# Optimization experiments

Measured on AMD Instinct MI355X. Metric: run time of the kernel, lower is better.

Reference implementation:

```python
import jax, jax.numpy as jnp
import numpy as np

L = 5        # num GNN layers
H = 256      # hidden size
N = 200000   # total nodes in batch
E = 400000   # total edges
G = 8000     # number of graphs (25 nodes each)


def _gelu(x):
    return jax.nn.gelu(x, approximate=False)


def _ln(x, g, b, eps=1e-5):
    m = x.mean(-1, keepdims=True)
    v = ((x - m) ** 2).mean(-1, keepdims=True)
    return (x - m) / jnp.sqrt(v + eps) * g + b


def _mlp(x, w1, b1, g, bb, w2, b2):
    # Linear -> LayerNorm -> GELU -> Linear (dropout is identity in eval)
    h = x @ w1 + b1
    h = _ln(h, g, bb)
    h = _gelu(h)
    return h @ w2 + b2


def setup_inputs() -> dict:
    key = jax.random.key(0)
    ks = jax.random.split(key, 24)
    s = 0.02
    inp = {}
    inp['x'] = jax.random.randint(ks[0], (N,), 0, 118)
    inp['edge_index'] = jax.random.randint(ks[1], (2, E), 0, N)
    inp['edge_attr'] = jax.random.randint(ks[2], (E,), 0, 5)
    # deterministic sorted graph ids: 25 nodes per graph, all G graphs nonempty
    inp['batch'] = jnp.arange(N, dtype=jnp.int32) // (N // G)
    # embeddings
    inp['atom_emb'] = jax.random.normal(ks[3], (118, H), jnp.float32) * s
    inp['vn_emb'] = jnp.zeros((1, H), jnp.float32)  # init constant 0
    inp['bond_emb'] = jax.random.normal(ks[4], (L, 5, H), jnp.float32) * s
    inp['eps'] = jnp.zeros((L,), jnp.float32)
    # GINConv mlp params (stacked over layers)
    inp['c_w1'] = jax.random.normal(ks[5], (L, H, 4 * H), jnp.float32) * s
    inp['c_b1'] = jnp.zeros((L, 4 * H), jnp.float32)
    inp['c_lng'] = jnp.ones((L, 4 * H), jnp.float32)
    inp['c_lnb'] = jnp.zeros((L, 4 * H), jnp.float32)
    inp['c_w2'] = jax.random.normal(ks[6], (L, 4 * H, H), jnp.float32) * s
    inp['c_b2'] = jnp.zeros((L, H), jnp.float32)
    # per-layer output LayerNorms
    inp['n_g'] = jnp.ones((L, H), jnp.float32)
    inp['n_b'] = jnp.zeros((L, H), jnp.float32)
    # virtual-node MLPs (L-1 of them)
    inp['v_w1'] = jax.random.normal(ks[7], (L - 1, H, 4 * H), jnp.float32) * s
    inp['v_b1'] = jnp.zeros((L - 1, 4 * H), jnp.float32)
    inp['v_lng'] = jnp.ones((L - 1, 4 * H), jnp.float32)
    inp['v_lnb'] = jnp.zeros((L - 1, 4 * H), jnp.float32)
    inp['v_w2'] = jax.random.normal(ks[8], (L - 1, 4 * H, H), jnp.float32) * s
    inp['v_b2'] = jnp.zeros((L - 1, H), jnp.float32)
    # projection head
    inp['p_w1'] = jax.random.normal(ks[9], (H, H), jnp.float32) * s
    inp['p_b1'] = jnp.zeros((H,), jnp.float32)
    inp['p_lng'] = jnp.ones((H,), jnp.float32)
    inp['p_lnb'] = jnp.zeros((H,), jnp.float32)
    inp['p_w2'] = jax.random.normal(ks[10], (H, H), jnp.float32) * s
    inp['p_b2'] = jnp.zeros((H,), jnp.float32)
    return inp


def reference(x, edge_index, edge_attr, batch, atom_emb, vn_emb, bond_emb, eps,
              c_w1, c_b1, c_lng, c_lnb, c_w2, c_b2, n_g, n_b,
              v_w1, v_b1, v_lng, v_lnb, v_w2, v_b2,
              p_w1, p_b1, p_lng, p_lnb, p_w2, p_b2):
    src, dst = edge_index[0], edge_index[1]
    vn = jnp.broadcast_to(vn_emb[0], (G, H))  # virtualnode embedding per graph
    h = atom_emb[x]                            # [N, H]
    for l in range(L):
        h = h + vn[batch]
        h_in = h
        # GINConv: gather + add + gelu per edge, scatter-add at dst
        edge_e = bond_emb[l][edge_attr]        # [E, H]
        msg = _gelu(h[src] + edge_e)           # [E, H]
        aggr = jax.ops.segment_sum(msg, dst, num_segments=N)
        out = _mlp((1.0 + eps[l]) * h + aggr,
                   c_w1[l], c_b1[l], c_lng[l], c_lnb[l], c_w2[l], c_b2[l])
        out = _ln(out, n_g[l], n_b[l])
        if l < L - 1:
            out = _gelu(out)
        h = out + h_in                         # residual
        if l < L - 1:
            vp = jax.ops.segment_max(h_in, batch, num_segments=G)
            vn = vn + _mlp(vp, v_w1[l], v_b1[l], v_lng[l], v_lnb[l], v_w2[l], v_b2[l])
    h_graph = jax.ops.segment_sum(h, batch, num_segments=G)  # [G, H]
    z = h_graph @ p_w1 + p_b1
    z = _gelu(_ln(z, p_lng, p_lnb))
    z = z @ p_w2 + p_b2
    z = z / jnp.linalg.norm(z, axis=-1, keepdims=True)
    return z
```

## Files before the change

### kernel.cpp

```cpp
#include <hip/hip_runtime.h>
#include <math.h>

typedef __bf16 bf16_t;
typedef __bf16 bfrag  __attribute__((ext_vector_type(8)));
typedef __bf16 b4     __attribute__((ext_vector_type(4)));
typedef __bf16 b2v    __attribute__((ext_vector_type(2)));
typedef float  f32x4  __attribute__((ext_vector_type(4)));

static constexpr int LY  = 5;
static constexpr int H   = 256;
static constexpr int NN  = 200000;
static constexpr int EE  = 400000;
static constexpr int GG  = 8000;
static constexpr int NPG = 25;
static constexpr int CAP = 24;
static constexpr int NBLK_NODE = NN / 32;
static constexpr int NBLK_VN   = GG / 32;

__device__ __forceinline__ float gelu_f(float x) {
    const float y = 0.7978845608028654f * x * (1.0f + 0.044715f * x * x);
    const float e = __expf(2.0f * y);
    const float t = 1.0f - 2.0f / (e + 1.0f);
    return 0.5f * x * (1.0f + t);
}

__global__ void k_fill(float* __restrict__ out, float v, int n) {
    const int i = blockIdx.x * 256 + threadIdx.x;
    if (i < n) out[i] = v;
}

__global__ void k_detect(const void* __restrict__ probe, int* __restrict__ flag) {
    const bf16_t* p = (const bf16_t*)probe;
    int bad = 0;
    for (int i = threadIdx.x; i < 256; i += 64) {
        const float v = (float)p[i];
        if (!(v == v) || fabsf(v) > 1000.0f) bad = 1;
    }
    const int any = __any(bad) ? 1 : 0;
    if (threadIdx.x == 0) *flag = any;
}

struct CvtJobs {
    const void* src[18];
    bf16_t*     dst[18];
    int         pfx[19];
    int         njobs;
};
__global__ void k_cvt_all(CvtJobs J, const int* __restrict__ flag) {
    const int i = blockIdx.x * 256 + threadIdx.x;
    if (i >= J.pfx[J.njobs]) return;
    int j = 0;
    while (i >= J.pfx[j + 1]) ++j;
    const int loc = i - J.pfx[j];
    if (*flag) J.dst[j][loc] = (bf16_t)((const float*)J.src[j])[loc];
    else       J.dst[j][loc] = ((const bf16_t*)J.src[j])[loc];
}

struct TpJobs {
    const void* s32[22];
    const void* s16[22];
    bf16_t*     dst[22];
    int R[22], C[22];
    int pfx[23];
    int njobs;
};
__global__ void k_tp_all(TpJobs J, const int* __restrict__ flag) {
    __shared__ bf16_t t[32][33];
    const int tile = blockIdx.x;
    int j = 0;
    while (tile >= J.pfx[j + 1]) ++j;
    const int tl = tile - J.pfx[j];
    const int C = J.C[j], R = J.R[j];
    const int ntx = C / 32;
    const int c0 = (tl % ntx) * 32, r0 = (tl / ntx) * 32;
    const int f = *flag;
    const int tx = threadIdx.x & 31, ty = threadIdx.x >> 5;
    #pragma unroll
    for (int i = 0; i < 4; ++i) {
        const int r = ty + i * 8;
        const size_t idx = (size_t)(r0 + r) * C + c0 + tx;
        t[r][tx] = f ? (bf16_t)((const float*)J.s32[j])[idx] : ((const bf16_t*)J.s16[j])[idx];
    }
    __syncthreads();
    #pragma unroll
    for (int i = 0; i < 4; ++i) {
        const int r = ty + i * 8;
        J.dst[j][(size_t)(c0 + r) * R + r0 + tx] = t[tx][r];
    }
}

__global__ void k_init_h(const int* __restrict__ x, const bf16_t* __restrict__ atom,
                         bf16_t* __restrict__ h) {
    const size_t idx = (size_t)blockIdx.x * 256 + threadIdx.x;
    const int row = (int)(idx >> 8), col = (int)(idx & 255);
    h[idx] = atom[(size_t)x[row] * H + col];
}

__global__ void k_init_vn(const bf16_t* __restrict__ vne, float* __restrict__ vn) {
    const size_t idx = (size_t)blockIdx.x * 256 + threadIdx.x;
    vn[idx] = (float)vne[idx & 255];
}

__global__ void k_zero_cnt(int* __restrict__ cnt) {
    const int i = blockIdx.x * 256 + threadIdx.x;
    if (i < NN) cnt[i] = 0;
}
// ... 2 lines not shown
                         int* __restrict__ cnt, int* __restrict__ slots) {
    const int e = blockIdx.x * 256 + threadIdx.x;
    if (e >= EE) return;
    const int d = ei[EE + e];
    const int s = ei[e];
    const int a = ea[e];
    const int slot = atomicAdd(&cnt[d], 1);
    if (slot < CAP) slots[(size_t)d * CAP + slot] = s | (a << 18);
}

__global__ void k_addvn_segmax(bf16_t* __restrict__ h, const float* __restrict__ vn,
                               bf16_t* __restrict__ vp, int do_max) {
    const int g = blockIdx.x, t = threadIdx.x;
    const float2 v = *(const float2*)(vn + (size_t)g * H + 2 * t);
    float mx0 = -1e30f, mx1 = -1e30f;
    #pragma unroll 5
    for (int i = 0; i < NPG; ++i) {
        bf16_t* p = h + ((size_t)g * NPG + i) * H + 2 * t;
        const b2v hv = *(const b2v*)p;
        const float h0 = (float)hv[0] + v.x;
        const float h1 = (float)hv[1] + v.y;
        b2v o; o[0] = (bf16_t)h0; o[1] = (bf16_t)h1;
        *(b2v*)p = o;
        mx0 = fmaxf(mx0, h0); mx1 = fmaxf(mx1, h1);
    }
    if (do_max) {
        b2v o; o[0] = (bf16_t)mx0; o[1] = (bf16_t)mx1;
        *(b2v*)(vp + (size_t)g * H + 2 * t) = o;
    }
}

__global__ void k_gather(const bf16_t* __restrict__ h,
                         const bf16_t* __restrict__ bondl,
                         const int* __restrict__ cnt, const int* __restrict__ slots,
                         const bf16_t* __restrict__ epsb, int l, bf16_t* __restrict__ Xb) {
    const int n = blockIdx.x, t = threadIdx.x;
    int deg = cnt[n];
    if (deg > CAP) deg = CAP;
    float m0 = 0.0f, m1 = 0.0f;
    for (int i = 0; i < deg; ++i) {
        const int p = slots[(size_t)n * CAP + i];
        const int s = p & 0x3FFFF;
        const int a = p >> 18;
        const b2v hv = *(const b2v*)(h + (size_t)s * H + 2 * t);
        const b2v bv = *(const b2v*)(bondl + (size_t)a * H + 2 * t);
        m0 += gelu_f((float)hv[0] + (float)bv[0]);
        m1 += gelu_f((float)hv[1] + (float)bv[1]);
    }
    const float eps1 = 1.0f + (float)epsb[l];
    const b2v hn = *(const b2v*)(h + (size_t)n * H + 2 * t);
    b2v o;
    o[0] = (bf16_t)(eps1 * (float)hn[0] + m0);
    o[1] = (bf16_t)(eps1 * (float)hn[1] + m1);
    *(b2v*)(Xb + (size_t)n * H + 2 * t) = o;
}

__global__ void k_graphsum(const bf16_t* __restrict__ h, bf16_t* __restrict__ hg) {
    const int g = blockIdx.x, t = threadIdx.x;
    float s0 = 0.0f, s1 = 0.0f;
    #pragma unroll 5
    for (int i = 0; i < NPG; ++i) {
        const b2v hv = *(const b2v*)(h + ((size_t)g * NPG + i) * H + 2 * t);
        s0 += (float)hv[0]; s1 += (float)hv[1];
    }
    b2v o; o[0] = (bf16_t)s0; o[1] = (bf16_t)s1;
    *(b2v*)(hg + (size_t)g * H + 2 * t) = o;
}

__global__ void k_norm(const float* __restrict__ z, float* __restrict__ out) {
    const int row = blockIdx.x, t = threadIdx.x;
    const size_t idx = (size_t)row * H + t;
    const float v = z[idx];
    float q = v * v;
    #pragma unroll
    for (int o = 32; o > 0; o >>= 1) q += __shfl_xor(q, o, 64);
    __shared__ float rq[4];
    const int wave = t >> 6, lane = t & 63;
    if (lane == 0) rq[wave] = q;
    __syncthreads();
    q = rq[0] + rq[1] + rq[2] + rq[3];
    out[idx] = v * rsqrtf(q);
}

__launch_bounds__(512, 4)
__global__ void k_mlp_dual(const bf16_t* __restrict__ Xn, const bf16_t* __restrict__ Xv,
                           const bf16_t* __restrict__ nW1T, const bf16_t* __restrict__ vW1T,
                           const bf16_t* __restrict__ nb1, const bf16_t* __restrict__ vb1,
                           const bf16_t* __restrict__ nlng, const bf16_t* __restrict__ vlng,
                           const bf16_t* __restrict__ nlnb, const bf16_t* __restrict__ vlnb,
                           const bf16_t* __restrict__ nW2T, const bf16_t* __restrict__ vW2T,
                           const bf16_t* __restrict__ nb2, const bf16_t* __restrict__ vb2,
                           const bf16_t* __restrict__ g2, const bf16_t* __restrict__ b2ln,
                           bf16_t* __restrict__ hres, float* __restrict__ vnacc,
                           int gelu_flag, int nblk_node, int has_vn) {
    constexpr int HID = 1024;
    constexpr int NP1 = HID / 128;
    constexpr int NQ2 = HID / 64;
    __shared__ bf16_t hid[32 * HID];
    __shared__ bf16_t wbuf[8192];
    const int tid  = threadIdx.x;
    const int lane = tid & 63, wave = tid >> 6;
    const int c16  = lane & 15, quad = lane >> 4;

    const bool is_node = (int)blockIdx.x < nblk_node;
    const size_t rowblk = is_node ? (size_t)blockIdx.x * 32
                                  : (size_t)((int)blockIdx.x - nblk_node) * 32;
    const bf16_t* X    = is_node ? Xn   : Xv;
    const bf16_t* W1T  = is_node ? nW1T : vW1T;
    const bf16_t* W2T  = is_node ? nW2T : vW2T;
    const bf16_t* b1   = is_node ? nb1  : vb1;
    const bf16_t* lng  = is_node ? nlng : vlng;
    const bf16_t* lnb  = is_node ? nlnb : vlnb;
    const bf16_t* b2   = is_node ? nb2  : vb2;

    auto stage = [&](const bf16_t* WT, int KW, int colbase, int k0) {
        #pragma unroll
        for (int j = 0; j < 2; ++j) {
            const int grp    = wave * 2 + j;
            const int colrel = grp * 8 + (lane >> 3);
            const int slot   = lane & 7;
            const int kq     = slot ^ (colrel & 7);
            const bf16_t* gp = WT + (size_t)(colbase + colrel) * KW + k0 + kq * 8;
            bf16_t* lp = &wbuf[(size_t)grp * 512];
            __builtin_amdgcn_global_load_lds(
                (const __attribute__((address_space(1))) void*)gp,
                (__attribute__((address_space(3))) void*)lp, 16, 0, 0);
        }
    };
    auto wfrag = [&](int crel, int g) -> bfrag {
        return *(const bfrag*)(wbuf + crel * 64 + ((g ^ (crel & 7)) * 8));
    };

    const bf16_t* xr0 = X + (rowblk + c16) * 256 + quad * 8;
    const bf16_t* xr1 = X + (rowblk + 16 + c16) * 256 + quad * 8;
    bfrag xa[8][2];
    #pragma unroll
    for (int ks = 0; ks < 8; ++ks) {
        xa[ks][0] = *(const bfrag*)(xr0 + ks * 32);
        xa[ks][1] = *(const bfrag*)(xr1 + ks * 32);
    }

    #pragma unroll
    for (int c = 0; c < NP1; ++c) {
        const int nbase = c * 128 + wave * 16;
        f32x4 acc[2];
        acc[0] = f32x4{0.f, 0.f, 0.f, 0.f};
        acc[1] = f32x4{0.f, 0.f, 0.f, 0.f};
        #pragma unroll
        for (int kc = 0; kc < 4; ++kc) {
            stage(W1T, 256, c * 128, kc * 64);
            __syncthreads();
            #pragma unroll
            for (int s = 0; s < 2; ++s) {
                const int ks = kc * 2 + s;
                const int g  = s * 4 + quad;
                const bfrag w0 = wfrag(wave * 16 + c16, g);
                #pragma unroll
                for (int mt = 0; mt < 2; ++mt)
                    acc[mt] = __builtin_amdgcn_mfma_f32_16x16x32_bf16(
                        w0, xa[ks][mt], acc[mt], 0, 0, 0);
            }
            __syncthreads();
        }
        #pragma unroll
        for (int mt = 0; mt < 2; ++mt) {
            const int kb = nbase + quad * 4;
            const int xr = mt * 16 + c16;
            const b4 bias = *(const b4*)(b1 + kb);
            b4 o;
            #pragma unroll
            for (int r = 0; r < 4; ++r)
                o[r] = (bf16_t)(acc[mt][r] + (float)bias[r]);
            const int ch = ((kb >> 3) ^ (xr & 7));
            *(b4*)(hid + xr * HID + ch * 8 + (kb & 7)) = o;
        }
    }
    __syncthreads();

    {
        const int row = tid >> 4, p = tid & 15;
        float sum = 0.f, ss = 0.f;
        #pragma unroll
        for (int i = 0; i < HID / 128; ++i) {
            const int j0 = p * 8 + i * 128;
            const int ch = ((j0 >> 3) ^ (row & 7));
            bfrag v = *(const bfrag*)(hid + row * HID + ch * 8);
            #pragma unroll
            for (int k = 0; k < 8; ++k) { const float f = (float)v[k]; sum += f; ss += f * f; }
        }
        #pragma unroll
        for (int o = 1; o < 16; o <<= 1) { sum += __shfl_xor(sum, o, 64); ss += __shfl_xor(ss, o, 64); }
        const float mean = sum * (1.0f / HID);
        const float var  = ss * (1.0f / HID) - mean * mean;
        const float rinv = rsqrtf(var + 1e-5f);
        #pragma unroll
        for (int i = 0; i < HID / 128; ++i) {
            const int j0 = p * 8 + i * 128;
            const int ch = ((j0 >> 3) ^ (row & 7));
            bfrag v  = *(const bfrag*)(hid + row * HID + ch * 8);
            bfrag gv = *(const bfrag*)(lng + j0);
            bfrag bv = *(const bfrag*)(lnb + j0);
            bfrag o8;
            #pragma unroll
            for (int k = 0; k < 8; ++k) {
                const float f = ((float)v[k] - mean) * rinv * (float)gv[k] + (float)bv[k];
                o8[k] = (bf16_t)gelu_f(f);
            }
            *(bfrag*)(hid + row * HID + ch * 8) = o8;
        }
    }
    __syncthreads();

    {
        f32x4 acc2[2][2];
        #pragma unroll
        for (int cp = 0; cp < 2; ++cp)
            #pragma unroll
            for (int mt = 0; mt < 2; ++mt)
                acc2[cp][mt] = f32x4{0.f, 0.f, 0.f, 0.f};
        #pragma unroll
        for (int cp = 0; cp < 2; ++cp) {
            for (int q2 = 0; q2 < NQ2; ++q2) {
                stage(W2T, HID, cp * 128, q2 * 64);
                __syncthreads();
                #pragma unroll
                for (int s = 0; s < 2; ++s) {
                    const int g = s * 4 + quad;
                    const bfrag w0 = wfrag(wave * 16 + c16, g);
                    const int k = q2 * 64 + s * 32 + quad * 8;
                    bfrag hb[2];
                    #pragma unroll
                    for (int mt = 0; mt < 2; ++mt) {
                        const int row = mt * 16 + c16;
                        const int ch = ((k >> 3) ^ (row & 7));
                        hb[mt] = *(const bfrag*)(hid + row * HID + ch * 8);
                    }
                    #pragma unroll
                    for (int mt = 0; mt < 2; ++mt)
                        acc2[cp][mt] = __builtin_amdgcn_mfma_f32_16x16x32_bf16(
                            w0, hb[mt], acc2[cp][mt], 0, 0, 0);
                }
                __syncthreads();
            }
        }

        if (!is_node) {
            if (has_vn) {
                #pragma unroll
                for (int cp = 0; cp < 2; ++cp)
                    #pragma unroll
                    for (int mt = 0; mt < 2; ++mt) {
                        const int cb = cp * 128 + wave * 16 + quad * 4;
                        const b4 b2vv = *(const b4*)(b2 + cb);
                        float* po = vnacc + (rowblk + mt * 16 + c16) * 256 + cb;
                        const f32x4 old = *(const f32x4*)po;
                        f32x4 v;
                        #pragma unroll
                        for (int r = 0; r < 4; ++r) v[r] = old[r] + acc2[cp][mt][r] + (float)b2vv[r];
                        *(f32x4*)po = v;
                    }
            }
        } else {
            constexpr int OS = 260;
            float* ot = (float*)hid;
            __syncthreads();
            #pragma unroll
            for (int cp = 0; cp < 2; ++cp)
                #pragma unroll
                for (int mt = 0; mt < 2; ++mt) {
                    const int cb = cp * 128 + wave * 16 + quad * 4;
                    const b4 b2vv = *(const b4*)(b2 + cb);
                    f32x4 v;
                    #pragma unroll
                    for (int r = 0; r < 4; ++r) v[r] = acc2[cp][mt][r] + (float)b2vv[r];
                    *(f32x4*)(ot + (mt * 16 + c16) * OS + cb) = v;
                }
            __syncthreads();
            const int row = tid >> 4, p = tid & 15;
            float s = 0.f, q = 0.f;
            #pragma unroll
            for (int i = 0; i < 16; ++i) {
                const float f = ot[row * OS + p + 16 * i];
                s += f; q += f * f;
            }
            #pragma unroll
            for (int o = 1; o < 16; o <<= 1) { s += __shfl_xor(s, o, 64); q += __shfl_xor(q, o, 64); }
            const float mean = s * (1.0f / 256.0f);
            const float var  = q * (1.0f / 256.0f) - mean * mean;
            const float rinv = rsqrtf(var + 1e-5f);
            const size_t rg = (rowblk + row) * 256;
            #pragma unroll
            for (int i = 0; i < 2; ++i) {
                const int j0 = p * 16 + i * 8;
                bfrag gv = *(const bfrag*)(g2 + j0);
                bfrag bv = *(const bfrag*)(b2ln + j0);
                bfrag hv = *(const bfrag*)(hres + rg + j0);
                bfrag o8;
                #pragma unroll
                for (int k = 0; k < 8; ++k) {
                    float f = (ot[row * OS + j0 + k] - mean) * rinv * (float)gv[k] + (float)bv[k];
                    if (gelu_flag) f = gelu_f(f);
                    o8[k] = (bf16_t)(f + (float)hv[k]);
                }
                *(bfrag*)(hres + rg + j0) = o8;
            }
        }
    }
}

__launch_bounds__(512, 4)
__global__ void k_mlp_proj(const bf16_t* __restrict__ X, const bf16_t* __restrict__ W1T,
                           const bf16_t* __restrict__ b1, const bf16_t* __restrict__ lng,
                           const bf16_t* __restrict__ lnb, const bf16_t* __restrict__ W2T,
                           const bf16_t* __restrict__ b2, float* __restrict__ outf) {
    constexpr int HID = 256;
    constexpr int NP1 = HID / 128;
    constexpr int NQ2 = HID / 64;
    __shared__ bf16_t hid[32 * HID];
    __shared__ bf16_t wbuf[8192];
    const int tid  = threadIdx.x;
    const int lane = tid & 63, wave = tid >> 6;
    const int c16  = lane & 15, quad = lane >> 4;
    const size_t rowblk = (size_t)blockIdx.x * 32;

    auto stage = [&](const bf16_t* WT, int KW, int colbase, int k0) {
        #pragma unroll
        for (int j = 0; j < 2; ++j) {
            const int grp    = wave * 2 + j;
            const int colrel = grp * 8 + (lane >> 3);
            const int slot   = lane & 7;
            const int kq     = slot ^ (colrel & 7);
            const bf16_t* gp = WT + (size_t)(colbase + colrel) * KW + k0 + kq * 8;
            bf16_t* lp = &wbuf[(size_t)grp * 512];
            __builtin_amdgcn_global_load_lds(
                (const __attribute__((address_space(1))) void*)gp,
                (__attribute__((address_space(3))) void*)lp, 16, 0, 0);
        }
    };
    auto wfrag = [&](int crel, int g) -> bfrag {
        return *(const bfrag*)(wbuf + crel * 64 + ((g ^ (crel & 7)) * 8));
    };

    const bf16_t* xr0 = X + (rowblk + c16) * 256 + quad * 8;
    const bf16_t* xr1 = X + (rowblk + 16 + c16) * 256 + quad * 8;
    bfrag xa[8][2];
    #pragma unroll
    for (int ks = 0; ks < 8; ++ks) {
        xa[ks][0] = *(const bfrag*)(xr0 + ks * 32);
        xa[ks][1] = *(const bfrag*)(xr1 + ks * 32);
    }

    #pragma unroll
    for (int c = 0; c < NP1; ++c) {
        const int nbase = c * 128 + wave * 16;
        f32x4 acc[2];
        acc[0] = f32x4{0.f, 0.f, 0.f, 0.f};
        acc[1] = f32x4{0.f, 0.f, 0.f, 0.f};
        #pragma unroll
        for (int kc = 0; kc < 4; ++kc) {
            stage(W1T, 256, c * 128, kc * 64);
            __syncthreads();
            #pragma unroll
            for (int s = 0; s < 2; ++s) {
                const int ks = kc * 2 + s;
                const int g  = s * 4 + quad;
                const bfrag w0 = wfrag(wave * 16 + c16, g);
                #pragma unroll
                for (int mt = 0; mt < 2; ++mt)
                    acc[mt] = __builtin_amdgcn_mfma_f32_16x16x32_bf16(
                        w0, xa[ks][mt], acc[mt], 0, 0, 0);
            }
            __syncthreads();
        }
        #pragma unroll
        for (int mt = 0; mt < 2; ++mt) {
            const int kb = nbase + quad * 4;
            const int xr = mt * 16 + c16;
            const b4 bias = *(const b4*)(b1 + kb);
            b4 o;
            #pragma unroll
            for (int r = 0; r < 4; ++r)
                o[r] = (bf16_t)(acc[mt][r] + (float)bias[r]);
            const int ch = ((kb >> 3) ^ (xr & 7));
            *(b4*)(hid + xr * HID + ch * 8 + (kb & 7)) = o;
        }
    }
    __syncthreads();

    {
        const int row = tid >> 4, p = tid & 15;
        float sum = 0.f, ss = 0.f;
        #pragma unroll
        for (int i = 0; i < HID / 128; ++i) {
            const int j0 = p * 8 + i * 128;
            const int ch = ((j0 >> 3) ^ (row & 7));
            bfrag v = *(const bfrag*)(hid + row * HID + ch * 8);
            #pragma unroll
            for (int k = 0; k < 8; ++k) { const float f = (float)v[k]; sum += f; ss += f * f; }
        }
        #pragma unroll
        for (int o = 1; o < 16; o <<= 1) { sum += __shfl_xor(sum, o, 64); ss += __shfl_xor(ss, o, 64); }
        const float mean = sum * (1.0f / HID);
        const float var  = ss * (1.0f / HID) - mean * mean;
        const float rinv = rsqrtf(var + 1e-5f);
        #pragma unroll
        for (int i = 0; i < HID / 128; ++i) {
            const int j0 = p * 8 + i * 128;
            const int ch = ((j0 >> 3) ^ (row & 7));
            bfrag v  = *(const bfrag*)(hid + row * HID + ch * 8);
            bfrag gv = *(const bfrag*)(lng + j0);
            bfrag bv = *(const bfrag*)(lnb + j0);
            bfrag o8;
            #pragma unroll
            for (int k = 0; k < 8; ++k) {
                const float f = ((float)v[k] - mean) * rinv * (float)gv[k] + (float)bv[k];
                o8[k] = (bf16_t)gelu_f(f);
            }
            *(bfrag*)(hid + row * HID + ch * 8) = o8;
        }
    }
    __syncthreads();

    {
        f32x4 acc2[2][2];
        #pragma unroll
        for (int cp = 0; cp < 2; ++cp)
            #pragma unroll
            for (int mt = 0; mt < 2; ++mt)
                acc2[cp][mt] = f32x4{0.f, 0.f, 0.f, 0.f};
        #pragma unroll
        for (int cp = 0; cp < 2; ++cp) {
            for (int q2 = 0; q2 < NQ2; ++q2) {
                stage(W2T, HID, cp * 128, q2 * 64);
                __syncthreads();
                #pragma unroll
                for (int s = 0; s < 2; ++s) {
                    const int g = s * 4 + quad;
                    const bfrag w0 = wfrag(wave * 16 + c16, g);
                    const int k = q2 * 64 + s * 32 + quad * 8;
                    bfrag hb[2];
                    #pragma unroll
                    for (int mt = 0; mt < 2; ++mt) {
                        const int row = mt * 16 + c16;
                        const int ch = ((k >> 3) ^ (row & 7));
                        hb[mt] = *(const bfrag*)(hid + row * HID + ch * 8);
                    }
                    #pragma unroll
                    for (int mt = 0; mt < 2; ++mt)
                        acc2[cp][mt] = __builtin_amdgcn_mfma_f32_16x16x32_bf16(
                            w0, hb[mt], acc2[cp][mt], 0, 0, 0);
                }
                __syncthreads();
            }
        }
        #pragma unroll
        for (int cp = 0; cp < 2; ++cp)
            #pragma unroll
            for (int mt = 0; mt < 2; ++mt) {
                const int cb = cp * 128 + wave * 16 + quad * 4;
                const b4 b2vv = *(const b4*)(b2 + cb);
                f32x4 v;
                #pragma unroll
                for (int r = 0; r < 4; ++r) v[r] = acc2[cp][mt][r] + (float)b2vv[r];
                *(f32x4*)(outf + (rowblk + mt * 16 + c16) * 256 + cb) = v;
            }
    }
}

extern "C" void kernel_launch(void* const* d_in, const int* in_sizes, int n_in,
                              void* d_out, int out_size, void* d_ws, size_t ws_size,
                              hipStream_t stream) {
    float* outz = (float*)d_out;

    const bool layout_ok =
        (n_in == 28) &&
        in_sizes[0] == 200000 && in_sizes[1] == 800000 &&
        in_sizes[2] == 400000 && in_sizes[3] == 200000 &&
        in_sizes[4] == 118 * 256 && in_sizes[6] == 5 * 5 * 256 &&
        in_sizes[8] == 5 * 256 * 1024 && in_sizes[27] == 256 &&
        out_size == GG * H;
    if (!layout_ok) {
        k_fill<<<(out_size + 255) / 256, 256, 0, stream>>>(outz, 777.0f, out_size);
        return;
    }

    char* w = (char*)d_ws;
    size_t off = 0;
    auto alloc = [&](size_t bytes) -> void* {
        void* p = w + off;
        off += (bytes + 255) & ~(size_t)255;
        return p;
    };
    bf16_t* h     = (bf16_t*)alloc((size_t)NN * H * 2);
    bf16_t* Xb    = (bf16_t*)alloc((size_t)NN * H * 2);
    float*  vn    = (float*) alloc((size_t)GG * H * 4);
    bf16_t* vpb   = (bf16_t*)alloc((size_t)GG * H * 2);
    bf16_t* hgb   = (bf16_t*)alloc((size_t)GG * H * 2);
    float*  pout2 = (float*) alloc((size_t)GG * H * 4);
    int*    cnt   = (int*)   alloc((size_t)NN * 4);
    int*    slots = (int*)   alloc((size_t)NN * CAP * 4);
    int*    dflag = (int*)   alloc(256);
    bf16_t* cw1T  = (bf16_t*)alloc((size_t)LY * 1024 * 256 * 2);
    bf16_t* cw2T  = (bf16_t*)alloc((size_t)LY * 256 * 1024 * 2);
    bf16_t* vw1T  = (bf16_t*)alloc((size_t)(LY - 1) * 1024 * 256 * 2);
    bf16_t* vw2T  = (bf16_t*)alloc((size_t)(LY - 1) * 256 * 1024 * 2);
    bf16_t* pw1T  = (bf16_t*)alloc((size_t)256 * 256 * 2);
    bf16_t* pw2T  = (bf16_t*)alloc((size_t)256 * 256 * 2);
    bf16_t* atomA = (bf16_t*)alloc((size_t)118 * 256 * 2);
    bf16_t* vneA  = (bf16_t*)alloc(256 * 2);
    bf16_t* bondA = (bf16_t*)alloc((size_t)LY * 5 * 256 * 2);
    bf16_t* epsA  = (bf16_t*)alloc(16 * 2);
    bf16_t* cb1A  = (bf16_t*)alloc((size_t)LY * 1024 * 2);
    bf16_t* clngA = (bf16_t*)alloc((size_t)LY * 1024 * 2);
    bf16_t* clnbA = (bf16_t*)alloc((size_t)LY * 1024 * 2);
    bf16_t* cb2A  = (bf16_t*)alloc((size_t)LY * 256 * 2);
    bf16_t* ngA   = (bf16_t*)alloc((size_t)LY * 256 * 2);
    bf16_t* nbA   = (bf16_t*)alloc((size_t)LY * 256 * 2);
    bf16_t* vb1A  = (bf16_t*)alloc((size_t)(LY - 1) * 1024 * 2);
    bf16_t* vlngA = (bf16_t*)alloc((size_t)(LY - 1) * 1024 * 2);
    bf16_t* vlnbA = (bf16_t*)alloc((size_t)(LY - 1) * 1024 * 2);
    bf16_t* vb2A  = (bf16_t*)alloc((size_t)(LY - 1) * 256 * 2);
    bf16_t* pb1A  = (bf16_t*)alloc(256 * 2);
    bf16_t* plngA = (bf16_t*)alloc(256 * 2);
    bf16_t* plnbA = (bf16_t*)alloc(256 * 2);
    bf16_t* pb2A  = (bf16_t*)alloc(256 * 2);
    if (off > ws_size) {
        k_fill<<<(out_size + 255) / 256, 256, 0, stream>>>(outz, 333.0f, out_size);
        return;
    }

    const int* xi  = (const int*)d_in[0];
    const int* ei  = (const int*)d_in[1];
    const int* ea  = (const int*)d_in[2];

    k_detect<<<1, 64, 0, stream>>>(d_in[8], dflag);
// ... 77 lines not shown
```

Measured before the change: 4.093 ms.

## Load MLP weight fragments directly from global memory instead of staging through LDS

In both fused MLP kernels, each wave now reads its MFMA weight fragments straight from global memory (L2/L1-cached) rather than cooperatively staging 64-wide K slices into an LDS buffer. This removes the per-slice __syncthreads pairs and frees 16KB of shared memory per block, which can allow higher occupancy. In exchange, each wave issues uncoalesced 16-byte global loads with exposed latency and no cross-wave sharing through LDS, so performance now depends on cache hit rates for the weights.

```diff
diff --git a/kernel.cpp b/kernel.cpp
--- a/kernel.cpp
+++ b/kernel.cpp
@@ -203,9 +203,7 @@
                            int gelu_flag, int nblk_node, int has_vn) {
     constexpr int HID = 1024;
     constexpr int NP1 = HID / 128;
-    constexpr int NQ2 = HID / 64;
     __shared__ bf16_t hid[32 * HID];
-    __shared__ bf16_t wbuf[8192];
     const int tid  = threadIdx.x;
     const int lane = tid & 63, wave = tid >> 6;
     const int c16  = lane & 15, quad = lane >> 4;
@@ -221,24 +219,6 @@
     const bf16_t* lnb  = is_node ? nlnb : vlnb;
     const bf16_t* b2   = is_node ? nb2  : vb2;
 
-    auto stage = [&](const bf16_t* WT, int KW, int colbase, int k0) {
-        #pragma unroll
-        for (int j = 0; j < 2; ++j) {
-            const int grp    = wave * 2 + j;
-            const int colrel = grp * 8 + (lane >> 3);
-            const int slot   = lane & 7;
-            const int kq     = slot ^ (colrel & 7);
-            const bf16_t* gp = WT + (size_t)(colbase + colrel) * KW + k0 + kq * 8;
-            bf16_t* lp = &wbuf[(size_t)grp * 512];
-            __builtin_amdgcn_global_load_lds(
-                (const __attribute__((address_space(1))) void*)gp,
-                (__attribute__((address_space(3))) void*)lp, 16, 0, 0);
-        }
-    };
-    auto wfrag = [&](int crel, int g) -> bfrag {
-        return *(const bfrag*)(wbuf + crel * 64 + ((g ^ (crel & 7)) * 8));
-    };
-
     const bf16_t* xr0 = X + (rowblk + c16) * 256 + quad * 8;
     const bf16_t* xr1 = X + (rowblk + 16 + c16) * 256 + quad * 8;
     bfrag xa[8][2];
@@ -248,39 +228,33 @@
         xa[ks][1] = *(const bfrag*)(xr1 + ks * 32);
     }
 
-    #pragma unroll
-    for (int c = 0; c < NP1; ++c) {
-        const int nbase = c * 128 + wave * 16;
-        f32x4 acc[2];
-        acc[0] = f32x4{0.f, 0.f, 0.f, 0.f};
-        acc[1] = f32x4{0.f, 0.f, 0.f, 0.f};
-        #pragma unroll
-        for (int kc = 0; kc < 4; ++kc) {
-            stage(W1T, 256, c * 128, kc * 64);
-            __syncthreads();
-            #pragma unroll
-            for (int s = 0; s < 2; ++s) {
-                const int ks = kc * 2 + s;
-                const int g  = s * 4 + quad;
-                const bfrag w0 = wfrag(wave * 16 + c16, g);
-                #pragma unroll
-                for (int mt = 0; mt < 2; ++mt)
-                    acc[mt] = __builtin_amdgcn_mfma_f32_16x16x32_bf16(
-                        w0, xa[ks][mt], acc[mt], 0, 0, 0);
-            }
-            __syncthreads();
-        }
-        #pragma unroll
-        for (int mt = 0; mt < 2; ++mt) {
-            const int kb = nbase + quad * 4;
-            const int xr = mt * 16 + c16;
-            const b4 bias = *(const b4*)(b1 + kb);
-            b4 o;
-            #pragma unroll
-            for (int r = 0; r < 4; ++r)
-                o[r] = (bf16_t)(acc[mt][r] + (float)bias[r]);
-            const int ch = ((kb >> 3) ^ (xr & 7));
-            *(b4*)(hid + xr * HID + ch * 8 + (kb & 7)) = o;
+    {
+        const bf16_t* w1l = W1T + (size_t)(wave * 16 + c16) * 256 + quad * 8;
+        #pragma unroll
+        for (int c = 0; c < NP1; ++c) {
+            const bf16_t* wp = w1l + (size_t)c * 128 * 256;
+            f32x4 acc[2];
+            acc[0] = f32x4{0.f, 0.f, 0.f, 0.f};
+            acc[1] = f32x4{0.f, 0.f, 0.f, 0.f};
+            #pragma unroll
+            for (int ks = 0; ks < 8; ++ks) {
+                const bfrag w0 = *(const bfrag*)(wp + ks * 32);
+                acc[0] = __builtin_amdgcn_mfma_f32_16x16x32_bf16(w0, xa[ks][0], acc[0], 0, 0, 0);
+                acc[1] = __builtin_amdgcn_mfma_f32_16x16x32_bf16(w0, xa[ks][1], acc[1], 0, 0, 0);
+            }
+            const int nbase = c * 128 + wave * 16;
+            #pragma unroll
+            for (int mt = 0; mt < 2; ++mt) {
+                const int kb = nbase + quad * 4;
+                const int xr = mt * 16 + c16;
+                const b4 bias = *(const b4*)(b1 + kb);
+                b4 o;
+                #pragma unroll
+                for (int r = 0; r < 4; ++r)
+                    o[r] = (bf16_t)(acc[mt][r] + (float)bias[r]);
+                const int ch = ((kb >> 3) ^ (xr & 7));
+                *(b4*)(hid + xr * HID + ch * 8 + (kb & 7)) = o;
+            }
         }
     }
     __syncthreads();
@@ -326,29 +300,25 @@
             #pragma unroll
             for (int mt = 0; mt < 2; ++mt)
                 acc2[cp][mt] = f32x4{0.f, 0.f, 0.f, 0.f};
+        const bf16_t* w2l = W2T + (size_t)(wave * 16 + c16) * HID + quad * 8;
         #pragma unroll
         for (int cp = 0; cp < 2; ++cp) {
-            for (int q2 = 0; q2 < NQ2; ++q2) {
-                stage(W2T, HID, cp * 128, q2 * 64);
-                __syncthreads();
-                #pragma unroll
-                for (int s = 0; s < 2; ++s) {
-                    const int g = s * 4 + quad;
-                    const bfrag w0 = wfrag(wave * 16 + c16, g);
-                    const int k = q2 * 64 + s * 32 + quad * 8;
-                    bfrag hb[2];
-                    #pragma unroll
-                    for (int mt = 0; mt < 2; ++mt) {
-                        const int row = mt * 16 + c16;
-                        const int ch = ((k >> 3) ^ (row & 7));
-                        hb[mt] = *(const bfrag*)(hid + row * HID + ch * 8);
-                    }
-                    #pragma unroll
-                    for (int mt = 0; mt < 2; ++mt)
-                        acc2[cp][mt] = __builtin_amdgcn_mfma_f32_16x16x32_bf16(
-                            w0, hb[mt], acc2[cp][mt], 0, 0, 0);
+            const bf16_t* wp = w2l + (size_t)cp * 128 * HID;
+            #pragma unroll 4
+            for (int kt = 0; kt < HID / 32; ++kt) {
+                const bfrag w0 = *(const bfrag*)(wp + kt * 32);
+                const int k = kt * 32 + quad * 8;
+                bfrag hb[2];
+                #pragma unroll
+                for (int mt = 0; mt < 2; ++mt) {
+                    const int row = mt * 16 + c16;
+                    const int ch = ((k >> 3) ^ (row & 7));
+                    hb[mt] = *(const bfrag*)(hid + row * HID + ch * 8);
                 }
-                __syncthreads();
+                #pragma unroll
+                for (int mt = 0; mt < 2; ++mt)
+                    acc2[cp][mt] = __builtin_amdgcn_mfma_f32_16x16x32_bf16(
+                        w0, hb[mt], acc2[cp][mt], 0, 0, 0);
             }
         }
 
@@ -423,31 +393,11 @@
                            const bf16_t* __restrict__ b2, float* __restrict__ outf) {
     constexpr int HID = 256;
     constexpr int NP1 = HID / 128;
-    constexpr int NQ2 = HID / 64;
     __shared__ bf16_t hid[32 * HID];
-    __shared__ bf16_t wbuf[8192];
     const int tid  = threadIdx.x;
     const int lane = tid & 63, wave = tid >> 6;
     const int c16  = lane & 15, quad = lane >> 4;
     const size_t rowblk = (size_t)blockIdx.x * 32;
-
-    auto stage = [&](const bf16_t* WT, int KW, int colbase, int k0) {
-        #pragma unroll
-        for (int j = 0; j < 2; ++j) {
-            const int grp    = wave * 2 + j;
-            const int colrel = grp * 8 + (lane >> 3);
-            const int slot   = lane & 7;
-            const int kq     = slot ^ (colrel & 7);
-            const bf16_t* gp = WT + (size_t)(colbase + colrel) * KW + k0 + kq * 8;
-            bf16_t* lp = &wbuf[(size_t)grp * 512];
-            __builtin_amdgcn_global_load_lds(
-                (const __attribute__((address_space(1))) void*)gp,
-                (__attribute__((address_space(3))) void*)lp, 16, 0, 0);
-        }
-    };
-    auto wfrag = [&](int crel, int g) -> bfrag {
-        return *(const bfrag*)(wbuf + crel * 64 + ((g ^ (crel & 7)) * 8));
-    };
 
     const bf16_t* xr0 = X + (rowblk + c16) * 256 + quad * 8;
     const bf16_t* xr1 = X + (rowblk + 16 + c16) * 256 + quad * 8;
@@ -458,39 +408,33 @@
         xa[ks][1] = *(const bfrag*)(xr1 + ks * 32);
     }
 
-    #pragma unroll
-    for (int c = 0; c < NP1; ++c) {
-        const int nbase = c * 128 + wave * 16;
-        f32x4 acc[2];
-        acc[0] = f32x4{0.f, 0.f, 0.f, 0.f};
-        acc[1] = f32x4{0.f, 0.f, 0.f, 0.f};
-        #pragma unroll
-        for (int kc = 0; kc < 4; ++kc) {
-            stage(W1T, 256, c * 128, kc * 64);
-            __syncthreads();
-            #pragma unroll
-            for (int s = 0; s < 2; ++s) {
-                const int ks = kc * 2 + s;
-                const int g  = s * 4 + quad;
-                const bfrag w0 = wfrag(wave * 16 + c16, g);
-                #pragma unroll
-                for (int mt = 0; mt < 2; ++mt)
-                    acc[mt] = __builtin_amdgcn_mfma_f32_16x16x32_bf16(
-                        w0, xa[ks][mt], acc[mt], 0, 0, 0);
-            }
-            __syncthreads();
-        }
-        #pragma unroll
-        for (int mt = 0; mt < 2; ++mt) {
-            const int kb = nbase + quad * 4;
-            const int xr = mt * 16 + c16;
-            const b4 bias = *(const b4*)(b1 + kb);
-            b4 o;
-            #pragma unroll
-            for (int r = 0; r < 4; ++r)
-                o[r] = (bf16_t)(acc[mt][r] + (float)bias[r]);
-            const int ch = ((kb >> 3) ^ (xr & 7));
-            *(b4*)(hid + xr * HID + ch * 8 + (kb & 7)) = o;
+    {
+        const bf16_t* w1l = W1T + (size_t)(wave * 16 + c16) * 256 + quad * 8;
+        #pragma unroll
+        for (int c = 0; c < NP1; ++c) {
+            const bf16_t* wp = w1l + (size_t)c * 128 * 256;
+            f32x4 acc[2];
+            acc[0] = f32x4{0.f, 0.f, 0.f, 0.f};
+            acc[1] = f32x4{0.f, 0.f, 0.f, 0.f};
+            #pragma unroll
+            for (int ks = 0; ks < 8; ++ks) {
+                const bfrag w0 = *(const bfrag*)(wp + ks * 32);
+                acc[0] = __builtin_amdgcn_mfma_f32_16x16x32_bf16(w0, xa[ks][0], acc[0], 0, 0, 0);
+                acc[1] = __builtin_amdgcn_mfma_f32_16x16x32_bf16(w0, xa[ks][1], acc[1], 0, 0, 0);
+            }
+            const int nbase = c * 128 + wave * 16;
+            #pragma unroll
+            for (int mt = 0; mt < 2; ++mt) {
+                const int kb = nbase + quad * 4;
+                const int xr = mt * 16 + c16;
+                const b4 bias = *(const b4*)(b1 + kb);
+                b4 o;
+                #pragma unroll
+                for (int r = 0; r < 4; ++r)
+                    o[r] = (bf16_t)(acc[mt][r] + (float)bias[r]);
+                const int ch = ((kb >> 3) ^ (xr & 7));
+                *(b4*)(hid + xr * HID + ch * 8 + (kb & 7)) = o;
+            }
         }
     }
     __syncthreads();
@@ -536,29 +480,25 @@
             #pragma unroll
             for (int mt = 0; mt < 2; ++mt)
                 acc2[cp][mt] = f32x4{0.f, 0.f, 0.f, 0.f};
+        const bf16_t* w2l = W2T + (size_t)(wave * 16 + c16) * HID + quad * 8;
         #pragma unroll
         for (int cp = 0; cp < 2; ++cp) {
-            for (int q2 = 0; q2 < NQ2; ++q2) {
-                stage(W2T, HID, cp * 128, q2 * 64);
-                __syncthreads();
-                #pragma unroll
-                for (int s = 0; s < 2; ++s) {
-                    const int g = s * 4 + quad;
-                    const bfrag w0 = wfrag(wave * 16 + c16, g);
-                    const int k = q2 * 64 + s * 32 + quad * 8;
-                    bfrag hb[2];
-                    #pragma unroll
-                    for (int mt = 0; mt < 2; ++mt) {
-                        const int row = mt * 16 + c16;
-                        const int ch = ((k >> 3) ^ (row & 7));
-                        hb[mt] = *(const bfrag*)(hid + row * HID + ch * 8);
-                    }
-                    #pragma unroll
-                    for (int mt = 0; mt < 2; ++mt)
-                        acc2[cp][mt] = __builtin_amdgcn_mfma_f32_16x16x32_bf16(
-                            w0, hb[mt], acc2[cp][mt], 0, 0, 0);
+            const bf16_t* wp = w2l + (size_t)cp * 128 * HID;
+            #pragma unroll
+            for (int kt = 0; kt < HID / 32; ++kt) {
+                const bfrag w0 = *(const bfrag*)(wp + kt * 32);
+                const int k = kt * 32 + quad * 8;
+                bfrag hb[2];
+                #pragma unroll
+                for (int mt = 0; mt < 2; ++mt) {
+                    const int row = mt * 16 + c16;
+                    const int ch = ((k >> 3) ^ (row & 7));
+                    hb[mt] = *(const bfrag*)(hid + row * HID + ch * 8);
                 }
-                __syncthreads();
+                #pragma unroll
+                for (int mt = 0; mt < 2; ++mt)
+                    acc2[cp][mt] = __builtin_amdgcn_mfma_f32_16x16x32_bf16(
+                        w0, hb[mt], acc2[cp][mt], 0, 0, 0);
             }
         }
         #pragma unroll
```

New measurement: 5.559 ms. 1.36x slower.

## Software-pipeline weight staging in dual MLP kernel with 4-deep LDS ring

Applied to the files above, without the earlier changes.

Replaces the single weight staging buffer and the two block barriers per k-chunk with a 4-slot LDS ring. Each round prefetches two rounds ahead with global_load_lds and uses one barrier gated by a partial vmcnt wait. Weight loads for W1 and W2 now overlap the MFMA work, and half the barriers disappear. Shared memory per block rises from 80 KB to 128 KB and launch bounds drop to 2 blocks per CU, which lowers occupancy. Relying on raw vmcnt counts for correctness is fragile, since the compiler may emit other vector memory ops that change the counts.

```diff
diff --git a/kernel.cpp b/kernel.cpp
--- a/kernel.cpp
+++ b/kernel.cpp
@@ -22,6 +22,31 @@
     const float e = __expf(2.0f * y);
     const float t = 1.0f - 2.0f / (e + 1.0f);
     return 0.5f * x * (1.0f + t);
+}
+
+__device__ __forceinline__ void pipe_bar_v4() {
+    asm volatile("s_waitcnt vmcnt(4)" ::: "memory");
+    __builtin_amdgcn_sched_barrier(0);
+    __builtin_amdgcn_s_barrier();
+    __builtin_amdgcn_sched_barrier(0);
+}
+__device__ __forceinline__ void pipe_bar_v2() {
+    asm volatile("s_waitcnt vmcnt(2)" ::: "memory");
+    __builtin_amdgcn_sched_barrier(0);
+    __builtin_amdgcn_s_barrier();
+    __builtin_amdgcn_sched_barrier(0);
+}
+__device__ __forceinline__ void pipe_bar_v0() {
+    asm volatile("s_waitcnt vmcnt(0)" ::: "memory");
+    __builtin_amdgcn_sched_barrier(0);
+    __builtin_amdgcn_s_barrier();
+    __builtin_amdgcn_sched_barrier(0);
+}
+__device__ __forceinline__ void lds_bar() {
+    asm volatile("s_waitcnt lgkmcnt(0)" ::: "memory");
+    __builtin_amdgcn_sched_barrier(0);
+    __builtin_amdgcn_s_barrier();
+    __builtin_amdgcn_sched_barrier(0);
 }
 
 __global__ void k_fill(float* __restrict__ out, float v, int n) {
@@ -190,7 +215,7 @@
     out[idx] = v * rsqrtf(q);
 }
 
-__launch_bounds__(512, 4)
+__launch_bounds__(512, 2)
 __global__ void k_mlp_dual(const bf16_t* __restrict__ Xn, const bf16_t* __restrict__ Xv,
                            const bf16_t* __restrict__ nW1T, const bf16_t* __restrict__ vW1T,
                            const bf16_t* __restrict__ nb1, const bf16_t* __restrict__ vb1,
@@ -202,10 +227,8 @@
                            bf16_t* __restrict__ hres, float* __restrict__ vnacc,
                            int gelu_flag, int nblk_node, int has_vn) {
     constexpr int HID = 1024;
-    constexpr int NP1 = HID / 128;
-    constexpr int NQ2 = HID / 64;
-    __shared__ bf16_t hid[32 * HID];
-    __shared__ bf16_t wbuf[8192];
+    __shared__ __align__(16) bf16_t hid[32 * HID];
+    __shared__ __align__(16) bf16_t wbuf[4][8192];
     const int tid  = threadIdx.x;
     const int lane = tid & 63, wave = tid >> 6;
     const int c16  = lane & 15, quad = lane >> 4;
@@ -221,7 +244,7 @@
     const bf16_t* lnb  = is_node ? nlnb : vlnb;
     const bf16_t* b2   = is_node ? nb2  : vb2;
 
-    auto stage = [&](const bf16_t* WT, int KW, int colbase, int k0) {
+    auto stage_to = [&](const bf16_t* WT, int KW, int colbase, int k0, bf16_t* lpbase) {
         #pragma unroll
         for (int j = 0; j < 2; ++j) {
             const int grp    = wave * 2 + j;
@@ -229,14 +252,20 @@
             const int slot   = lane & 7;
             const int kq     = slot ^ (colrel & 7);
             const bf16_t* gp = WT + (size_t)(colbase + colrel) * KW + k0 + kq * 8;
-            bf16_t* lp = &wbuf[(size_t)grp * 512];
+            bf16_t* lp = lpbase + (size_t)grp * 512;
             __builtin_amdgcn_global_load_lds(
                 (const __attribute__((address_space(1))) void*)gp,
                 (__attribute__((address_space(3))) void*)lp, 16, 0, 0);
         }
     };
-    auto wfrag = [&](int crel, int g) -> bfrag {
-        return *(const bfrag*)(wbuf + crel * 64 + ((g ^ (crel & 7)) * 8));
+    auto stage_round = [&](int g) {
+        bf16_t* base = wbuf[g & 3];
+        if (g < 32) {
+            stage_to(W1T, 256, (g >> 2) * 128, (g & 3) * 64, base);
+        } else {
+            const int gg = g - 32;
+            stage_to(W2T, HID, (gg >> 4) * 128, (gg & 15) * 64, base);
+        }
     };
 
     const bf16_t* xr0 = X + (rowblk + c16) * 256 + quad * 8;
@@ -248,28 +277,31 @@
         xa[ks][1] = *(const bfrag*)(xr1 + ks * 32);
     }
 
+    stage_round(0);
+    stage_round(1);
+
     #pragma unroll
-    for (int c = 0; c < NP1; ++c) {
-        const int nbase = c * 128 + wave * 16;
+    for (int c = 0; c < 8; ++c) {
         f32x4 acc[2];
         acc[0] = f32x4{0.f, 0.f, 0.f, 0.f};
         acc[1] = f32x4{0.f, 0.f, 0.f, 0.f};
         #pragma unroll
         for (int kc = 0; kc < 4; ++kc) {
-            stage(W1T, 256, c * 128, kc * 64);
-            __syncthreads();
+            const int r = c * 4 + kc;
+            stage_round(r + 2);
+            pipe_bar_v4();
+            const bf16_t* sb = wbuf[r & 3];
             #pragma unroll
             for (int s = 0; s < 2; ++s) {
                 const int ks = kc * 2 + s;
-                const int g  = s * 4 + quad;
-                const bfrag w0 = wfrag(wave * 16 + c16, g);
-                #pragma unroll
-                for (int mt = 0; mt < 2; ++mt)
-                    acc[mt] = __builtin_amdgcn_mfma_f32_16x16x32_bf16(
-                        w0, xa[ks][mt], acc[mt], 0, 0, 0);
-            }
-            __syncthreads();
-        }
+                const int gq = s * 4 + quad;
+                const int crel = wave * 16 + c16;
+                const bfrag w0 = *(const bfrag*)(sb + crel * 64 + ((gq ^ (crel & 7)) * 8));
+                acc[0] = __builtin_amdgcn_mfma_f32_16x16x32_bf16(w0, xa[ks][0], acc[0], 0, 0, 0);
+                acc[1] = __builtin_amdgcn_mfma_f32_16x16x32_bf16(w0, xa[ks][1], acc[1], 0, 0, 0);
+            }
+        }
+        const int nbase = c * 128 + wave * 16;
         #pragma unroll
         for (int mt = 0; mt < 2; ++mt) {
             const int kb = nbase + quad * 4;
@@ -283,7 +315,7 @@
             *(b4*)(hid + xr * HID + ch * 8 + (kb & 7)) = o;
         }
     }
-    __syncthreads();
+    lds_bar();
 
     {
         const int row = tid >> 4, p = tid & 15;
@@ -317,7 +349,7 @@
             *(bfrag*)(hid + row * HID + ch * 8) = o8;
         }
     }
-    __syncthreads();
+    lds_bar();
 
     {
         f32x4 acc2[2][2];
@@ -328,13 +360,19 @@
                 acc2[cp][mt] = f32x4{0.f, 0.f, 0.f, 0.f};
         #pragma unroll
         for (int cp = 0; cp < 2; ++cp) {
-            for (int q2 = 0; q2 < NQ2; ++q2) {
-                stage(W2T, HID, cp * 128, q2 * 64);
-                __syncthreads();
+            #pragma unroll
+            for (int q2 = 0; q2 < 16; ++q2) {
+                const int g = 32 + cp * 16 + q2;
+                if (g + 2 <= 63) stage_round(g + 2);
+                if (g <= 61)      pipe_bar_v4();
+                else if (g == 62) pipe_bar_v2();
+                else              pipe_bar_v0();
+                const bf16_t* sb = wbuf[g & 3];
                 #pragma unroll
                 for (int s = 0; s < 2; ++s) {
-                    const int g = s * 4 + quad;
-                    const bfrag w0 = wfrag(wave * 16 + c16, g);
+                    const int gq = s * 4 + quad;
+                    const int crel = wave * 16 + c16;
+                    const bfrag w0 = *(const bfrag*)(sb + crel * 64 + ((gq ^ (crel & 7)) * 8));
                     const int k = q2 * 64 + s * 32 + quad * 8;
                     bfrag hb[2];
                     #pragma unroll
@@ -343,12 +381,9 @@
                         const int ch = ((k >> 3) ^ (row & 7));
                         hb[mt] = *(const bfrag*)(hid + row * HID + ch * 8);
                     }
-                    #pragma unroll
-                    for (int mt = 0; mt < 2; ++mt)
-                        acc2[cp][mt] = __builtin_amdgcn_mfma_f32_16x16x32_bf16(
-                            w0, hb[mt], acc2[cp][mt], 0, 0, 0);
+                    acc2[cp][0] = __builtin_amdgcn_mfma_f32_16x16x32_bf16(w0, hb[0], acc2[cp][0], 0, 0, 0);
+                    acc2[cp][1] = __builtin_amdgcn_mfma_f32_16x16x32_bf16(w0, hb[1], acc2[cp][1], 0, 0, 0);
                 }
-                __syncthreads();
             }
         }
 
```

New measurement: 4.475 ms. +9.3%, slower.

## Give each wave private double-buffered weight staging and drop block barriers in MLP GEMMs

Applied to the files above, without the earlier changes.

In the fused dual MLP kernel, weight tiles were staged cooperatively into shared LDS with __syncthreads around every k-chunk. Now each wave stages only the 16 weight columns it consumes into its own double-buffered LDS slot, prefetches the next tile with global_load_lds and waits with an explicit vmcnt, so block-wide barriers inside both GEMM loops go away. X fragments are streamed two at a time instead of held all at once, which lowers register pressure, and the biases are loaded once up front. The risk is that the hand-written vmcnt counts and the removed barriers must exactly match the outstanding loads, and there is less cross-wave reuse of staged data.

```diff
diff --git a/kernel.cpp b/kernel.cpp
--- a/kernel.cpp
+++ b/kernel.cpp
@@ -202,10 +202,8 @@
                            bf16_t* __restrict__ hres, float* __restrict__ vnacc,
                            int gelu_flag, int nblk_node, int has_vn) {
     constexpr int HID = 1024;
-    constexpr int NP1 = HID / 128;
-    constexpr int NQ2 = HID / 64;
-    __shared__ bf16_t hid[32 * HID];
-    __shared__ bf16_t wbuf[8192];
+    __shared__ __align__(16) bf16_t hid[32 * HID];
+    __shared__ __align__(16) bf16_t wbuf[8192];
     const int tid  = threadIdx.x;
     const int lane = tid & 63, wave = tid >> 6;
     const int c16  = lane & 15, quad = lane >> 4;
@@ -221,64 +219,72 @@
     const bf16_t* lnb  = is_node ? nlnb : vlnb;
     const bf16_t* b2   = is_node ? nb2  : vb2;
 
-    auto stage = [&](const bf16_t* WT, int KW, int colbase, int k0) {
-        #pragma unroll
-        for (int j = 0; j < 2; ++j) {
-            const int grp    = wave * 2 + j;
-            const int colrel = grp * 8 + (lane >> 3);
-            const int slot   = lane & 7;
-            const int kq     = slot ^ (colrel & 7);
-            const bf16_t* gp = WT + (size_t)(colbase + colrel) * KW + k0 + kq * 8;
-            bf16_t* lp = &wbuf[(size_t)grp * 512];
-            __builtin_amdgcn_global_load_lds(
-                (const __attribute__((address_space(1))) void*)gp,
-                (__attribute__((address_space(3))) void*)lp, 16, 0, 0);
-        }
+    bf16_t* wb = wbuf + wave * 1024;
+    const bf16_t* w1l = W1T + (size_t)(wave * 16 + c16) * 256  + quad * 8;
+    const bf16_t* w2l = W2T + (size_t)(wave * 16 + c16) * 1024 + quad * 8;
+
+    auto stage1 = [&](int hr) {
+        const bf16_t* gp = w1l + (size_t)(hr >> 3) * (128 * 256) + (hr & 7) * 32;
+        bf16_t* lp = wb + (hr & 1) * 512;
+        __builtin_amdgcn_global_load_lds(
+            (const __attribute__((address_space(1))) void*)gp,
+            (__attribute__((address_space(3))) void*)lp, 16, 0, 0);
     };
-    auto wfrag = [&](int crel, int g) -> bfrag {
-        return *(const bfrag*)(wbuf + crel * 64 + ((g ^ (crel & 7)) * 8));
+    auto stage2 = [&](int g) {
+        const bf16_t* gp = w2l + (size_t)(g >> 5) * (128 * 1024) + (g & 31) * 32;
+        bf16_t* lp = wb + (g & 1) * 512;
+        __builtin_amdgcn_global_load_lds(
+            (const __attribute__((address_space(1))) void*)gp,
+            (__attribute__((address_space(3))) void*)lp, 16, 0, 0);
     };
+
+    b4 bias1[8], bias2[2];
+    #pragma unroll
+    for (int c = 0; c < 8; ++c)
+        bias1[c] = *(const b4*)(b1 + c * 128 + wave * 16 + quad * 4);
+    #pragma unroll
+    for (int cp = 0; cp < 2; ++cp)
+        bias2[cp] = *(const b4*)(b2 + cp * 128 + wave * 16 + quad * 4);
 
     const bf16_t* xr0 = X + (rowblk + c16) * 256 + quad * 8;
     const bf16_t* xr1 = X + (rowblk + 16 + c16) * 256 + quad * 8;
-    bfrag xa[8][2];
+    bfrag xb0[2], xb1[2];
+
+    stage1(0);
+    xb0[0] = *(const bfrag*)(xr0);
+    xb1[0] = *(const bfrag*)(xr1);
+
     #pragma unroll
-    for (int ks = 0; ks < 8; ++ks) {
-        xa[ks][0] = *(const bfrag*)(xr0 + ks * 32);
-        xa[ks][1] = *(const bfrag*)(xr1 + ks * 32);
-    }
-
-    #pragma unroll
-    for (int c = 0; c < NP1; ++c) {
-        const int nbase = c * 128 + wave * 16;
-        f32x4 acc[2];
-        acc[0] = f32x4{0.f, 0.f, 0.f, 0.f};
-        acc[1] = f32x4{0.f, 0.f, 0.f, 0.f};
-        #pragma unroll
-        for (int kc = 0; kc < 4; ++kc) {
-            stage(W1T, 256, c * 128, kc * 64);
-            __syncthreads();
-            #pragma unroll
-            for (int s = 0; s < 2; ++s) {
-                const int ks = kc * 2 + s;
-                const int g  = s * 4 + quad;
-                const bfrag w0 = wfrag(wave * 16 + c16, g);
-                #pragma unroll
-                for (int mt = 0; mt < 2; ++mt)
-                    acc[mt] = __builtin_amdgcn_mfma_f32_16x16x32_bf16(
-                        w0, xa[ks][mt], acc[mt], 0, 0, 0);
-            }
-            __syncthreads();
-        }
+    for (int c = 0; c < 8; ++c) {
+        f32x4 acc0 = f32x4{0.f, 0.f, 0.f, 0.f};
+        f32x4 acc1 = f32x4{0.f, 0.f, 0.f, 0.f};
+        #pragma unroll
+        for (int ks = 0; ks < 8; ++ks) {
+            const int hr = c * 8 + ks;
+            if (hr < 63) {
+                stage1(hr + 1);
+                const int nk = (hr + 1) & 7;
+                xb0[(hr + 1) & 1] = *(const bfrag*)(xr0 + nk * 32);
+                xb1[(hr + 1) & 1] = *(const bfrag*)(xr1 + nk * 32);
+                asm volatile("s_waitcnt vmcnt(3)" ::: "memory");
+            } else {
+                stage2(0);
+                asm volatile("s_waitcnt vmcnt(1)" ::: "memory");
+            }
+            __builtin_amdgcn_sched_barrier(0);
+            const bfrag w0 = *(const bfrag*)(wb + (hr & 1) * 512 + lane * 8);
+            acc0 = __builtin_amdgcn_mfma_f32_16x16x32_bf16(w0, xb0[hr & 1], acc0, 0, 0, 0);
+            acc1 = __builtin_amdgcn_mfma_f32_16x16x32_bf16(w0, xb1[hr & 1], acc1, 0, 0, 0);
+        }
+        const int kb = c * 128 + wave * 16 + quad * 4;
         #pragma unroll
         for (int mt = 0; mt < 2; ++mt) {
-            const int kb = nbase + quad * 4;
             const int xr = mt * 16 + c16;
-            const b4 bias = *(const b4*)(b1 + kb);
+            const f32x4 a = mt ? acc1 : acc0;
             b4 o;
             #pragma unroll
             for (int r = 0; r < 4; ++r)
-                o[r] = (bf16_t)(acc[mt][r] + (float)bias[r]);
+                o[r] = (bf16_t)(a[r] + (float)bias1[c][r]);
             const int ch = ((kb >> 3) ^ (xr & 7));
             *(b4*)(hid + xr * HID + ch * 8 + (kb & 7)) = o;
         }
@@ -328,27 +334,27 @@
                 acc2[cp][mt] = f32x4{0.f, 0.f, 0.f, 0.f};
         #pragma unroll
         for (int cp = 0; cp < 2; ++cp) {
-            for (int q2 = 0; q2 < NQ2; ++q2) {
-                stage(W2T, HID, cp * 128, q2 * 64);
-                __syncthreads();
+            #pragma unroll
+            for (int kt = 0; kt < 32; ++kt) {
+                const int g = cp * 32 + kt;
+                if (g < 63) {
+                    stage2(g + 1);
+                    asm volatile("s_waitcnt vmcnt(1)" ::: "memory");
+                } else {
+                    asm volatile("s_waitcnt vmcnt(0)" ::: "memory");
+                }
+                __builtin_amdgcn_sched_barrier(0);
+                const bfrag w0 = *(const bfrag*)(wb + (g & 1) * 512 + lane * 8);
+                const int k = kt * 32 + quad * 8;
+                bfrag hb[2];
                 #pragma unroll
-                for (int s = 0; s < 2; ++s) {
-                    const int g = s * 4 + quad;
-                    const bfrag w0 = wfrag(wave * 16 + c16, g);
-                    const int k = q2 * 64 + s * 32 + quad * 8;
-                    bfrag hb[2];
-                    #pragma unroll
-                    for (int mt = 0; mt < 2; ++mt) {
-                        const int row = mt * 16 + c16;
-                        const int ch = ((k >> 3) ^ (row & 7));
-                        hb[mt] = *(const bfrag*)(hid + row * HID + ch * 8);
-                    }
-                    #pragma unroll
-                    for (int mt = 0; mt < 2; ++mt)
-                        acc2[cp][mt] = __builtin_amdgcn_mfma_f32_16x16x32_bf16(
-                            w0, hb[mt], acc2[cp][mt], 0, 0, 0);
+                for (int mt = 0; mt < 2; ++mt) {
+                    const int row = mt * 16 + c16;
+                    const int ch = ((k >> 3) ^ (row & 7));
+                    hb[mt] = *(const bfrag*)(hid + row * HID + ch * 8);
                 }
-                __syncthreads();
+                acc2[cp][0] = __builtin_amdgcn_mfma_f32_16x16x32_bf16(w0, hb[0], acc2[cp][0], 0, 0, 0);
+                acc2[cp][1] = __builtin_amdgcn_mfma_f32_16x16x32_bf16(w0, hb[1], acc2[cp][1], 0, 0, 0);
             }
         }
 
@@ -359,12 +365,11 @@
                     #pragma unroll
                     for (int mt = 0; mt < 2; ++mt) {
                         const int cb = cp * 128 + wave * 16 + quad * 4;
-                        const b4 b2vv = *(const b4*)(b2 + cb);
                         float* po = vnacc + (rowblk + mt * 16 + c16) * 256 + cb;
                         const f32x4 old = *(const f32x4*)po;
                         f32x4 v;
                         #pragma unroll
-                        for (int r = 0; r < 4; ++r) v[r] = old[r] + acc2[cp][mt][r] + (float)b2vv[r];
+                        for (int r = 0; r < 4; ++r) v[r] = old[r] + acc2[cp][mt][r] + (float)bias2[cp][r];
                         *(f32x4*)po = v;
                     }
             }
@@ -377,10 +382,9 @@
                 #pragma unroll
                 for (int mt = 0; mt < 2; ++mt) {
                     const int cb = cp * 128 + wave * 16 + quad * 4;
-                    const b4 b2vv = *(const b4*)(b2 + cb);
                     f32x4 v;
                     #pragma unroll
-                    for (int r = 0; r < 4; ++r) v[r] = acc2[cp][mt][r] + (float)b2vv[r];
+                    for (int r = 0; r < 4; ++r) v[r] = acc2[cp][mt][r] + (float)bias2[cp][r];
                     *(f32x4*)(ot + (mt * 16 + c16) * OS + cb) = v;
                 }
             __syncthreads();
```

Result: slower. 8.549 ms (+108.9%).
